# Performance work log

Hardware: AMD Instinct MI355X
Metric: run time of the kernel (lower is better)

The kernel has to match this reference:

```python
import jax, jax.numpy as jnp
import numpy as np

S, B, V, E, H, T = 512, 64, 100000, 128, 256, 64


def setup_inputs() -> dict:
    key = jax.random.key(0)
    ks = jax.random.split(key, 12)
    sc = 0.08  # small init scale for numerical stability
    return {
        "inputs": jax.random.randint(ks[0], (S, B), 0, V, dtype=jnp.int64),
        "emb": jax.random.normal(ks[1], (V, E), dtype=jnp.float32) * sc,
        "W_ih_f": jax.random.normal(ks[2], (4 * H, E), dtype=jnp.float32) * sc,
        "W_hh_f": jax.random.normal(ks[3], (4 * H, H), dtype=jnp.float32) * sc,
        "b_ih_f": jax.random.normal(ks[4], (4 * H,), dtype=jnp.float32) * sc,
        "b_hh_f": jax.random.normal(ks[5], (4 * H,), dtype=jnp.float32) * sc,
        "W_ih_b": jax.random.normal(ks[6], (4 * H, E), dtype=jnp.float32) * sc,
        "W_hh_b": jax.random.normal(ks[7], (4 * H, H), dtype=jnp.float32) * sc,
        "b_ih_b": jax.random.normal(ks[8], (4 * H,), dtype=jnp.float32) * sc,
        "b_hh_b": jax.random.normal(ks[9], (4 * H,), dtype=jnp.float32) * sc,
        "W_out": jax.random.normal(ks[10], (T, 2 * H), dtype=jnp.float32) * sc,
        "b_out": jax.random.normal(ks[11], (T,), dtype=jnp.float32) * sc,
    }


def _lstm_scan(x_proj, W_hh):
    # x_proj: [S, B, 4H] = input projection + biases (precomputed, hoisted out of scan)
    Bsz = x_proj.shape[1]
    Hd = W_hh.shape[1]
    h0 = jnp.zeros((Bsz, Hd), x_proj.dtype)
    c0 = jnp.zeros((Bsz, Hd), x_proj.dtype)

    def step(carry, xp):
        h, c = carry
        g = xp + h @ W_hh.T  # [B, 4H]
        i, f, gg, o = jnp.split(g, 4, axis=-1)  # PyTorch gate order: i, f, g, o
        i = jax.nn.sigmoid(i)
        f = jax.nn.sigmoid(f)
        gg = jnp.tanh(gg)
        o = jax.nn.sigmoid(o)
        c = f * c + i * gg
        h = o * jnp.tanh(c)
        return (h, c), h

    _, hs = jax.lax.scan(step, (h0, c0), x_proj)
    return hs  # [S, B, H]


def reference(inputs, emb, W_ih_f, W_hh_f, b_ih_f, b_hh_f,
              W_ih_b, W_hh_b, b_ih_b, b_hh_b, W_out, b_out):
    x = emb[inputs]  # [S, B, E] embedding gather
    # forward direction
    xf = jnp.einsum('sbe,ge->sbg', x, W_ih_f) + (b_ih_f + b_hh_f)
    hf = _lstm_scan(xf, W_hh_f)  # [S, B, H]
    # backward direction: run on time-reversed sequence, then reverse outputs
    xr = x[::-1]
    xb = jnp.einsum('sbe,ge->sbg', xr, W_ih_b) + (b_ih_b + b_hh_b)
    hb = _lstm_scan(xb, W_hh_b)[::-1]  # [S, B, H]
    hcat = jnp.concatenate([hf, hb], axis=-1)  # [S, B, 2H]
    return jnp.einsum('sbh,th->sbt', hcat, W_out) + b_out  # [S, B, T]
```

## Files before the change

kernel.cpp:

```cpp
#include <hip/hip_runtime.h>

#define S_LEN 512
#define BATCH 64
#define EDIM  128
#define HDIM  256
#define GDIM  1024
#define TDIM  64
#define NROW  32768
#define HSTR  264

typedef __attribute__((ext_vector_type(8))) short short8;
typedef __attribute__((ext_vector_type(4))) short short4v;
typedef __attribute__((ext_vector_type(4))) unsigned short us4;
typedef __attribute__((ext_vector_type(4))) float f32x4;
typedef unsigned long long ull;

__device__ __forceinline__ unsigned short f2bf(float f) {
  unsigned u = __float_as_uint(f);
  u += 0x7FFFu + ((u >> 16) & 1u);
  return (unsigned short)(u >> 16);
}
__device__ __forceinline__ float bf2f(unsigned short h) {
  return __uint_as_float(((unsigned)h) << 16);
}
__device__ __forceinline__ float sigm(float x) {
  float e = __expf(-x);
  return __builtin_amdgcn_rcpf(1.f + e);
}
__device__ __forceinline__ float tanh_(float x) {
  float e = __expf(2.f * x);
  return 1.f - 2.f * __builtin_amdgcn_rcpf(e + 1.f);
}

__global__ __launch_bounds__(256) void k_pack(
    const float* __restrict__ Whf, const float* __restrict__ Whb,
    unsigned short* __restrict__ wpk, int* __restrict__ flags) {
  const int fid = blockIdx.x * 256 + threadIdx.x;
  const int l = fid & 63;
  int rest = fid >> 6;
  const int gi = rest & 3;  rest >>= 2;
  const int kk = rest & 7;  rest >>= 3;
  const int w  = rest & 3;  rest >>= 2;
  const int ch = rest & 3;  rest >>= 2;
  const int dir = rest;
  const int q = l >> 4, cl = l & 15;
  const float* Wh = dir ? Whb : Whf;
  const int row = gi * 256 + ch * 64 + w * 16 + cl;
  const float* src = Wh + (size_t)row * HDIM + kk * 32 + q * 8;
  float4 v0 = *(const float4*)src;
  float4 v1 = *(const float4*)(src + 4);
  short8 t8;
  t8[0] = (short)f2bf(v0.x); t8[1] = (short)f2bf(v0.y);
  t8[2] = (short)f2bf(v0.z); t8[3] = (short)f2bf(v0.w);
  t8[4] = (short)f2bf(v1.x); t8[5] = (short)f2bf(v1.y);
  t8[6] = (short)f2bf(v1.z); t8[7] = (short)f2bf(v1.w);
  *(short8*)(wpk + (size_t)fid * 8) = t8;
  if (blockIdx.x == 0)
    for (int i = threadIdx.x; i < 512; i += 256) flags[i] = 0;
}

__global__ __launch_bounds__(512) void k_proj(
    const int* __restrict__ tok, const float* __restrict__ emb,
    const float* __restrict__ Wf, const float* __restrict__ bihf, const float* __restrict__ bhhf,
    const float* __restrict__ Wb, const float* __restrict__ bihb, const float* __restrict__ bhhb,
    unsigned short* __restrict__ xqf, unsigned short* __restrict__ xqb) {
  __shared__ short xt[256 * 136];
  const int tid = threadIdx.x;
  const int rowbase = blockIdx.x * 256;
  const int dir = blockIdx.y;
  const float* W  = dir ? Wb   : Wf;
  const float* bi = dir ? bihb : bihf;
  const float* bh = dir ? bhhb : bhhf;
  unsigned short* xq = dir ? xqb : xqf;

  for (int i = tid; i < 256 * 32; i += 512) {
    int row = i >> 5, c4 = (i & 31) << 2;
    int t = tok[rowbase + row];
    float4 v = *(const float4*)(emb + (size_t)t * EDIM + c4);
    short4v p;
    p.x = (short)f2bf(v.x); p.y = (short)f2bf(v.y);
    p.z = (short)f2bf(v.z); p.w = (short)f2bf(v.w);
    *(short4v*)&xt[row * 136 + c4] = p;
  }
  __syncthreads();

  const int w = tid >> 6, l = tid & 63, q = l >> 4, cl = l & 15;

  short8 a[2][4];
#pragma unroll
  for (int rt = 0; rt < 2; ++rt)
#pragma unroll
    for (int kk = 0; kk < 4; ++kk)
      a[rt][kk] = *(const short8*)&xt[((2 * w + rt) * 16 + cl) * 136 + kk * 32 + q * 8];

  for (int ct = 0; ct < 64; ++ct) {
    const int colg = ct * 16 + cl;
    short8 bw[4];
#pragma unroll
    for (int kk = 0; kk < 4; ++kk) {
      const float* wp = W + (size_t)colg * EDIM + kk * 32 + q * 8;
      float4 w0 = *(const float4*)wp;
      float4 w1 = *(const float4*)(wp + 4);
      short8 t8;
      t8[0] = (short)f2bf(w0.x); t8[1] = (short)f2bf(w0.y);
      t8[2] = (short)f2bf(w0.z); t8[3] = (short)f2bf(w0.w);
      t8[4] = (short)f2bf(w1.x); t8[5] = (short)f2bf(w1.y);
      t8[6] = (short)f2bf(w1.z); t8[7] = (short)f2bf(w1.w);
      bw[kk] = t8;
    }
    float bias = bi[colg] + bh[colg];
#pragma unroll
    for (int rt = 0; rt < 2; ++rt) {
      f32x4 acc = {bias, bias, bias, bias};
#pragma unroll
      for (int kk = 0; kk < 4; ++kk)
        acc = __builtin_amdgcn_mfma_f32_16x16x32_bf16(a[rt][kk], bw[kk], acc, 0, 0, 0);
      const int rowg = rowbase + (2 * w + rt) * 16 + q * 4;
      const int s = rowg >> 6, b0 = rowg & 63;
      us4 p;
      p[0] = f2bf(acc[0]); p[1] = f2bf(acc[1]);
      p[2] = f2bf(acc[2]); p[3] = f2bf(acc[3]);
      *(us4*)&xq[((size_t)s * GDIM + colg) * BATCH + b0] = p;
    }
  }
}

__global__ __launch_bounds__(256, 1) __attribute__((amdgpu_waves_per_eu(1, 1)))
void k_lstm(
    const unsigned short* __restrict__ wpk,
    const unsigned short* __restrict__ xqf, const unsigned short* __restrict__ xqb,
    unsigned short* __restrict__ hq, unsigned short* __restrict__ hx,
    int* __restrict__ flags) {
  __shared__ short hb0[16][HSTR];
  __shared__ short hb1[16][HSTR];
  const int tid = threadIdx.x;
  const int bx = blockIdx.x;
  const int dir = bx & 1, ch = (bx >> 1) & 3, bg = bx >> 3;
  const int bxb8 = bx & ~7;
  const int w = tid >> 6, l = tid & 63, q = l >> 4, cl = l & 15;
  const int brow = bg * 16 + q * 4;
  const int hcol = ch * 64 + w * 16 + cl;
  const char* xqB = (const char*)(dir ? xqb : xqf);
  const char* wlp = (const char*)wpk + (size_t)((dir * 4 + ch) * 4 + w) * 32768 + l * 16;
  char* hxB = (char*)hx;

  for (int i = tid; i < 16 * HSTR; i += 256) { ((short*)hb0)[i] = 0; ((short*)hb1)[i] = 0; }

  short8 wst[8][4];
#pragma unroll
  for (int kk = 0; kk < 8; ++kk)
#pragma unroll
    for (int gi = 0; gi < 4; ++gi)
      wst[kk][gi] = *(const short8*)(wlp + (kk * 4 + gi) * 1024);

  int xlane[4];
#pragma unroll
  for (int gi = 0; gi < 4; ++gi)
    xlane[gi] = ((gi * 256 + hcol) * BATCH + brow) * 2;
  const int hq_lbyte = (brow * 512 + dir * 256 + hcol) * 2;

  const int sd  = dir ? -(GDIM * BATCH * 2) : (GDIM * BATCH * 2);
  const int hsd = dir ? -(BATCH * 512 * 2)  : (BATCH * 512 * 2);
  const int s0 = dir ? (S_LEN - 1) : 0;
  int xoff    = s0 * (GDIM * BATCH * 2);
  int hq_soff = s0 * (BATCH * 512 * 2);

  const int hx_own = bx * 2048 + (w * 16 + cl) * 32 + q * 8;
  const int gc = tid >> 2, grg = tid & 3;

  us4 xp[4];
#pragma unroll
  for (int gi = 0; gi < 4; ++gi)
    xp[gi] = *(const us4*)(xqB + xoff + xlane[gi]);
  xoff += sd;

  float cst[4] = {0.f, 0.f, 0.f, 0.f};
  __syncthreads();

#define STEP4(RB, WB, PAR, T) {                                              \
    f32x4 acc[4];                                                            \
    const f32x4 zz = {0.f, 0.f, 0.f, 0.f};                                   \
    acc[0] = zz; acc[1] = zz; acc[2] = zz; acc[3] = zz;                      \
    _Pragma("unroll") for (int kk = 0; kk < 8; ++kk) {                       \
      short8 av = *(const short8*)&RB[cl][kk * 32 + q * 8];                  \
      _Pragma("unroll") for (int gi = 0; gi < 4; ++gi)                       \
        acc[gi] = __builtin_amdgcn_mfma_f32_16x16x32_bf16(av, wst[kk][gi], acc[gi], 0, 0, 0); \
    }                                                                        \
    ull hpack = 0;                                                           \
    _Pragma("unroll") for (int r = 0; r < 4; ++r) {                          \
      float gi_ = sigm(acc[0][r] + bf2f(xp[0][r]));                          \
      float gf  = sigm(acc[1][r] + bf2f(xp[1][r]));                          \
      float gg  = tanh_(acc[2][r] + bf2f(xp[2][r]));                         \
      float go  = sigm(acc[3][r] + bf2f(xp[3][r]));                          \
      float cn = gf * cst[r] + gi_ * gg;                                     \
      cst[r] = cn;                                                           \
      unsigned short hbv = f2bf(go * tanh_(cn));                             \
      WB[q * 4 + r][hcol] = (short)hbv;                                      \
      hpack |= (ull)hbv << (16 * r);                                         \
    }                                                                        \
    __hip_atomic_store((ull*)(hxB + (PAR) * 65536 + hx_own), hpack,          \
                       __ATOMIC_RELAXED, __HIP_MEMORY_SCOPE_AGENT);          \
    asm volatile("s_waitcnt vmcnt(0)" ::: "memory");                         \
    __builtin_amdgcn_s_barrier();                                            \
    asm volatile("" ::: "memory");                                           \
    if (tid == 0)                                                            \
      __hip_atomic_store(&flags[bx * 16], (T) + 1, __ATOMIC_RELAXED,         \
                         __HIP_MEMORY_SCOPE_AGENT);                          \
    asm volatile("" ::: "memory");                                           \
         \
    _Pragma("unroll") for (int r = 0; r < 4; ++r)                            \
      *(unsigned short*)((char*)hq + hq_soff + hq_lbyte + r * 1024) =        \
          (unsigned short)(hpack >> (16 * r));                               \
    hq_soff += hsd;                                                          \
    _Pragma("unroll") for (int p = 0; p < 3; ++p) {                          \
      const int pc = (p < ch) ? p : p + 1;                                   \
      const int pbx = bxb8 + pc * 2 + dir;                                   \
      while (__hip_atomic_load(&flags[pbx * 16], __ATOMIC_RELAXED,           \
                               __HIP_MEMORY_SCOPE_AGENT) < (T) + 1) {}       \
    }                                                                        \
    asm volatile("" ::: "memory");                                           \
    _Pragma("unroll") for (int p = 0; p < 3; ++p) {                          \
      const int pc = (p < ch) ? p : p + 1;                                   \
      const int pbx = bxb8 + pc * 2 + dir;                                   \
      ull v = __hip_atomic_load(                                             \
          (const ull*)(hxB + (PAR) * 65536 + pbx * 2048 + gc * 32 + grg * 8),\
          __ATOMIC_RELAXED, __HIP_MEMORY_SCOPE_AGENT);                       \
      _Pragma("unroll") for (int j = 0; j < 4; ++j)                          \
        WB[grg * 4 + j][pc * 64 + gc] = (short)(unsigned short)(v >> (16 * j)); \
    }                                                                        \
    _Pragma("unroll") for (int gi = 0; gi < 4; ++gi)                         \
      xp[gi] = *(const us4*)(xqB + xoff + xlane[gi]);                        \
    if ((T) < S_LEN - 2) xoff += sd;                                         \
    asm volatile("s_waitcnt lgkmcnt(0)\n\ts_barrier" ::: "memory");          \
  }

  for (int it = 0; it < S_LEN / 2; ++it) {
    const int t = 2 * it;
    STEP4(hb0, hb1, 0, t);
    STEP4(hb1, hb0, 1, t + 1);
  }
#undef STEP4
}

__global__ __launch_bounds__(256) void k_out(
    const unsigned short* __restrict__ hq, const float* __restrict__ Wo,
    const float* __restrict__ bo, float* __restrict__ out) {
  __shared__ short wlds[64 * 520];
  const int tid = threadIdx.x;
  for (int i = tid; i < 64 * 128; i += 256) {
    int row = i >> 7, c4 = (i & 127) << 2;
    float4 v = *(const float4*)(Wo + (size_t)row * 512 + c4);
    short4v p;
    p.x = (short)f2bf(v.x); p.y = (short)f2bf(v.y);
    p.z = (short)f2bf(v.z); p.w = (short)f2bf(v.w);
    *(short4v*)&wlds[row * 520 + c4] = p;
  }
  __syncthreads();

  const int w = tid >> 6, l = tid & 63, q = l >> 4, cl = l & 15;
  const int rtb = blockIdx.x * 64 + w * 16;

  short8 a[16];
#pragma unroll
  for (int kk = 0; kk < 16; ++kk)
    a[kk] = *(const short8*)&hq[(size_t)(rtb + cl) * 512 + kk * 32 + q * 8];

#pragma unroll
  for (int ct = 0; ct < 4; ++ct) {
    float bias = bo[ct * 16 + cl];
    f32x4 acc = {bias, bias, bias, bias};
#pragma unroll
    for (int kk = 0; kk < 16; ++kk) {
      short8 b = *(const short8*)&wlds[(ct * 16 + cl) * 520 + kk * 32 + q * 8];
      acc = __builtin_amdgcn_mfma_f32_16x16x32_bf16(a[kk], b, acc, 0, 0, 0);
    }
#pragma unroll
    for (int r = 0; r < 4; ++r)
      out[(size_t)(rtb + q * 4 + r) * TDIM + ct * 16 + cl] = acc[r];
  }
}

extern "C" void kernel_launch(void* const* d_in, const int* in_sizes, int n_in,
                              void* d_out, int out_size, void* d_ws, size_t ws_size,
                              hipStream_t stream) {
  const int*   tok  = (const int*)d_in[0];
  const float* emb  = (const float*)d_in[1];
  const float* Wihf = (const float*)d_in[2];
  const float* Whhf = (const float*)d_in[3];
  const float* bihf = (const float*)d_in[4];
  const float* bhhf = (const float*)d_in[5];
  const float* Wihb = (const float*)d_in[6];
  const float* Whhb = (const float*)d_in[7];
  const float* bihb = (const float*)d_in[8];
  const float* bhhb = (const float*)d_in[9];
  const float* Wo   = (const float*)d_in[10];
  const float* bo   = (const float*)d_in[11];
  float* out = (float*)d_out;

  char* ws = (char*)d_ws;
  unsigned short* xqf = (unsigned short*)ws;
  unsigned short* xqb = (unsigned short*)(ws + (size_t)NROW * GDIM * 2);
  unsigned short* hq  = (unsigned short*)(ws + (size_t)NROW * GDIM * 4);
  unsigned short* wpk   = (unsigned short*)d_out;
  unsigned short* hx    = (unsigned short*)((char*)d_out + (2u << 20));
  int*            flags = (int*)((char*)d_out + (4u << 20));

  k_pack<<<256, 256, 0, stream>>>(Whhf, Whhb, wpk, flags);
  k_proj<<<dim3(128, 2), 512, 0, stream>>>(tok, emb, Wihf, bihf, bhhf,
                                           Wihb, bihb, bhhb, xqf, xqb);
  k_lstm<<<32, 256, 0, stream>>>(wpk, xqf, xqb, hq, hx, flags);
  k_out<<<512, 256, 0, stream>>>(hq, Wo, bo, out);
}
```

Before: 1.965 ms.

## Transpose published hidden state for vector LDS writes and centralize flag polling

Each wave transposes its packed hidden outputs with two lane shuffles, so the exchange buffer is stored row-major. Consumers can then copy 8 bytes straight into one LDS row instead of doing four scattered 2-byte stores. Only three threads now poll the peer flags, followed by a workgroup barrier, instead of every thread spinning. The block-to-(dir, chunk, batch-group) mapping is also changed so the four peer blocks are contiguous. The cost is extra shuffles and an added barrier on the per-step critical path.

```diff
diff --git a/kernel.cpp b/kernel.cpp
--- a/kernel.cpp
+++ b/kernel.cpp
@@ -135,8 +135,8 @@
   __shared__ short hb1[16][HSTR];
   const int tid = threadIdx.x;
   const int bx = blockIdx.x;
-  const int dir = bx & 1, ch = (bx >> 1) & 3, bg = bx >> 3;
-  const int bxb8 = bx & ~7;
+  const int ch = bx & 3, bg = (bx >> 2) & 3, dir = bx >> 4;
+  const int bxb = bx & ~3;
   const int w = tid >> 6, l = tid & 63, q = l >> 4, cl = l & 15;
   const int brow = bg * 16 + q * 4;
   const int hcol = ch * 64 + w * 16 + cl;
@@ -165,8 +165,9 @@
   int xoff    = s0 * (GDIM * BATCH * 2);
   int hq_soff = s0 * (BATCH * 512 * 2);
 
-  const int hx_own = bx * 2048 + (w * 16 + cl) * 32 + q * 8;
-  const int gc = tid >> 2, grg = tid & 3;
+  const int hx_pub  = bx * 2048 + (q * 4 + (cl & 3)) * 128
+                      + (w * 16 + (cl >> 2) * 4) * 2;
+  const int hx_prow = (tid >> 4) * 128 + (tid & 15) * 8;
 
   us4 xp[4];
 #pragma unroll
@@ -198,8 +199,25 @@
       WB[q * 4 + r][hcol] = (short)hbv;                                      \
       hpack |= (ull)hbv << (16 * r);                                         \
     }                                                                        \
-    __hip_atomic_store((ull*)(hxB + (PAR) * 65536 + hx_own), hpack,          \
-                       __ATOMIC_RELAXED, __HIP_MEMORY_SCOPE_AGENT);          \
+        \
+    {                                                                        \
+      ull tsh = (ull)__shfl_xor((long long)hpack, 2);                        \
+      unsigned lox = (unsigned)hpack, hix = (unsigned)(hpack >> 32);         \
+      unsigned lot = (unsigned)tsh,   hit = (unsigned)(tsh >> 32);           \
+      unsigned a0 = (cl & 2) ? hit : lox;                                    \
+      unsigned a1 = (cl & 2) ? hix : lot;                                    \
+      ull x1 = (ull)a0 | ((ull)a1 << 32);                                    \
+      ull t1 = (ull)__shfl_xor((long long)x1, 1);                            \
+      unsigned blx = (unsigned)x1, bhx = (unsigned)(x1 >> 32);               \
+      unsigned blt = (unsigned)t1, bht = (unsigned)(t1 >> 32);               \
+      unsigned c0 = (cl & 1) ? ((blt >> 16) | (blx & 0xFFFF0000u))           \
+                             : ((blx & 0xFFFFu) | (blt << 16));              \
+      unsigned c1 = (cl & 1) ? ((bht >> 16) | (bhx & 0xFFFF0000u))           \
+                             : ((bhx & 0xFFFFu) | (bht << 16));              \
+      ull tpack = (ull)c0 | ((ull)c1 << 32);                                 \
+      __hip_atomic_store((ull*)(hxB + (PAR) * 65536 + hx_pub), tpack,        \
+                         __ATOMIC_RELAXED, __HIP_MEMORY_SCOPE_AGENT);        \
+    }                                                                        \
     asm volatile("s_waitcnt vmcnt(0)" ::: "memory");                         \
     __builtin_amdgcn_s_barrier();                                            \
     asm volatile("" ::: "memory");                                           \
@@ -207,26 +225,24 @@
       __hip_atomic_store(&flags[bx * 16], (T) + 1, __ATOMIC_RELAXED,         \
                          __HIP_MEMORY_SCOPE_AGENT);                          \
     asm volatile("" ::: "memory");                                           \
-         \
+        \
     _Pragma("unroll") for (int r = 0; r < 4; ++r)                            \
       *(unsigned short*)((char*)hq + hq_soff + hq_lbyte + r * 1024) =        \
           (unsigned short)(hpack >> (16 * r));                               \
     hq_soff += hsd;                                                          \
-    _Pragma("unroll") for (int p = 0; p < 3; ++p) {                          \
-      const int pc = (p < ch) ? p : p + 1;                                   \
-      const int pbx = bxb8 + pc * 2 + dir;                                   \
-      while (__hip_atomic_load(&flags[pbx * 16], __ATOMIC_RELAXED,           \
+    if (tid < 3) {                                                           \
+      const int pc = (tid < ch) ? tid : tid + 1;                             \
+      while (__hip_atomic_load(&flags[(bxb + pc) * 16], __ATOMIC_RELAXED,    \
                                __HIP_MEMORY_SCOPE_AGENT) < (T) + 1) {}       \
     }                                                                        \
+    __builtin_amdgcn_s_barrier();                                            \
     asm volatile("" ::: "memory");                                           \
     _Pragma("unroll") for (int p = 0; p < 3; ++p) {                          \
       const int pc = (p < ch) ? p : p + 1;                                   \
-      const int pbx = bxb8 + pc * 2 + dir;                                   \
       ull v = __hip_atomic_load(                                             \
-          (const ull*)(hxB + (PAR) * 65536 + pbx * 2048 + gc * 32 + grg * 8),\
+          (const ull*)(hxB + (PAR) * 65536 + (bxb + pc) * 2048 + hx_prow),   \
           __ATOMIC_RELAXED, __HIP_MEMORY_SCOPE_AGENT);                       \
-      _Pragma("unroll") for (int j = 0; j < 4; ++j)                          \
-        WB[grg * 4 + j][pc * 64 + gc] = (short)(unsigned short)(v >> (16 * j)); \
+      *(ull*)&WB[tid >> 4][pc * 64 + (tid & 15) * 4] = v;                    \
     }                                                                        \
     _Pragma("unroll") for (int gi = 0; gi < 4; ++gi)                         \
       xp[gi] = *(const us4*)(xqB + xoff + xlane[gi]);                        \
```

Result: faster. 1.897 ms (-3.5%).
